# Kernel optimization log

Measured on AMD Instinct MI355X. Metric: run time of the kernel, lower is better.

## Reference

```python
import jax, jax.numpy as jnp
import numpy as np

B, L, D, S = 4, 4096, 1024, 16
EPS = 1e-5  # nn.LayerNorm default


def setup_inputs() -> dict:
    key = jax.random.key(0)
    ks = jax.random.split(key, 8)
    s = 0.02
    return {
        "x_seq": jax.random.normal(ks[0], (B, L, D), jnp.float32),
        "h_prev": jnp.zeros((B, S), jnp.float32),
        "gamma": jnp.ones((D,), jnp.float32),
        "beta": jnp.zeros((D,), jnp.float32),
        "W_in": jax.random.normal(ks[1], (D, D), jnp.float32) * s,
        "b_in": jnp.zeros((D,), jnp.float32),
        "W_A": jax.random.normal(ks[2], (D, S), jnp.float32) * s,
        "b_A": jnp.zeros((S,), jnp.float32),
        "W_B": jax.random.normal(ks[3], (D, S), jnp.float32) * s,
        "b_B": jnp.zeros((S,), jnp.float32),
        "W_C": jax.random.normal(ks[4], (D, S), jnp.float32) * s,
        "b_C": jnp.zeros((S,), jnp.float32),
        "W_dt": jax.random.normal(ks[5], (D, 1), jnp.float32) * s,
        "b_dt": jnp.zeros((1,), jnp.float32),
        "W_out": jax.random.normal(ks[6], (D, D), jnp.float32) * s,
        "b_out": jnp.zeros((D,), jnp.float32),
    }


def _layernorm(x, gamma, beta):
    mu = jnp.mean(x, axis=-1, keepdims=True)
    var = jnp.mean(jnp.square(x - mu), axis=-1, keepdims=True)
    return (x - mu) * jax.lax.rsqrt(var + EPS) * gamma + beta


def reference(x_seq, h_prev, gamma, beta, W_in, b_in, W_A, b_A, W_B, b_B,
              W_C, b_C, W_dt, b_dt, W_out, b_out):
    # pre-scan projections (all batched over (B, L))
    x = _layernorm(x_seq, gamma, beta)
    x = jax.nn.silu(x @ W_in + b_in)                    # (B, L, D)
    log_A = -jax.nn.softplus(x @ W_A + b_A)             # (B, L, S)
    B_t = x @ W_B + b_B                                 # (B, L, S)
    C_t = x @ W_C + b_C                                 # (B, L, S)
    dt = jax.nn.softplus(x @ W_dt + b_dt)               # (B, L, 1)
    A_disc = jnp.exp(log_A * dt)                        # (B, L, S)
    u = jnp.mean(x, axis=-1, keepdims=True)             # (B, L, 1)
    Bu = (B_t * dt) * u                                 # (B, L, S)

    # selective scan: h_t = A_t * h_{t-1} + Bu_t  over time axis
    def step(h, inp):
        a_t, bu_t = inp
        h = a_t * h + bu_t
        return h, h

    h_final, hs = jax.lax.scan(
        step, h_prev,
        (jnp.swapaxes(A_disc, 0, 1), jnp.swapaxes(Bu, 0, 1)))
    hs = jnp.swapaxes(hs, 0, 1)                         # (B, L, S)

    y = jnp.sum(C_t * hs, axis=-1, keepdims=True)       # (B, L, 1)
    y_seq = (x * y) @ W_out + b_out + x_seq             # (B, L, D)
    return y_seq, h_final
```

## Files before the change

kernel.cpp:

```cpp
#include <hip/hip_runtime.h>

typedef unsigned short u16;
typedef unsigned int u32;
typedef __attribute__((ext_vector_type(8))) short short8;
typedef __attribute__((ext_vector_type(4))) float f32x4;

#define B_ 4
#define L_ 4096
#define D_ 1024
#define S_ 16
#define M_ (B_ * L_)

__device__ __forceinline__ float b2f(u16 h) {
    unsigned u = ((unsigned)h) << 16;
    return __builtin_bit_cast(float, u);
}
__device__ __forceinline__ u16 f2b(float f) {
    unsigned u = __builtin_bit_cast(unsigned, f);
    u += 0x7fffu + ((u >> 16) & 1u);
    return (u16)(u >> 16);
}
__device__ __forceinline__ float softplus_f(float z) {
    return z > 20.f ? z : log1pf(__expf(z));
}
__device__ __forceinline__ void gload16(const u16* g, const u16* l) {
    __builtin_amdgcn_global_load_lds(
        (const __attribute__((address_space(1))) u32*)g,
        (__attribute__((address_space(3))) u32*)l, 16, 0, 0);
}

__global__ __launch_bounds__(256) void transpose_to_bf16(
    const float* __restrict__ W0, u16* __restrict__ Wt0,
    const float* __restrict__ W1, u16* __restrict__ Wt1) {
    const float* W = blockIdx.z ? W1 : W0;
    u16* Wt = blockIdx.z ? Wt1 : Wt0;
    __shared__ float t[32][33];
    int bx = blockIdx.x, by = blockIdx.y;
    int x = threadIdx.x;
    for (int j = threadIdx.y; j < 32; j += 8)
        t[j][x] = W[(size_t)(by * 32 + j) * D_ + bx * 32 + x];
    __syncthreads();
    for (int j = threadIdx.y; j < 32; j += 8)
        Wt[(size_t)(bx * 32 + j) * D_ + by * 32 + x] = f2b(t[x][j]);
}

__global__ __launch_bounds__(256) void pack_wp(
    const float* __restrict__ WA, const float* __restrict__ WB,
    const float* __restrict__ WC, const float* __restrict__ Wdt,
    u16* __restrict__ Wp) {
    int idx = blockIdx.x * 256 + threadIdx.x;
    int s = idx >> 10, k = idx & 1023;
    float v;
    if (s < 16)       v = WA[k * 16 + s];
    else if (s < 32)  v = WB[k * 16 + (s - 16)];
    else if (s < 48)  v = WC[k * 16 + (s - 32)];
    else if (s == 48) v = Wdt[k];
    else if (s == 49) v = 1.0f / 1024.0f;
    else              v = 0.f;
    Wp[idx] = f2b(v);
}

__global__ __launch_bounds__(256) void ln_kernel(
    const float* __restrict__ x, const float* __restrict__ gamma,
    const float* __restrict__ beta, u16* __restrict__ out) {
    int row = blockIdx.x, tid = threadIdx.x;
    const float4 v = *(const float4*)&x[(size_t)row * D_ + tid * 4];
    float s = v.x + v.y + v.z + v.w;
    float q = v.x * v.x + v.y * v.y + v.z * v.z + v.w * v.w;
    for (int o = 32; o > 0; o >>= 1) { s += __shfl_down(s, o); q += __shfl_down(q, o); }
    __shared__ float ss[4], qq[4];
    int w = tid >> 6, lane = tid & 63;
    if (lane == 0) { ss[w] = s; qq[w] = q; }
    __syncthreads();
    if (tid == 0) {
        float S = ss[0] + ss[1] + ss[2] + ss[3];
        float Q = qq[0] + qq[1] + qq[2] + qq[3];
        float mu = S * (1.f / D_);
        float var = Q * (1.f / D_) - mu * mu;
        ss[0] = mu; qq[0] = rsqrtf(var + 1e-5f);
    }
    __syncthreads();
    float mu = ss[0], rs = qq[0];
    const float4 gv = *(const float4*)&gamma[tid * 4];
    const float4 bv = *(const float4*)&beta[tid * 4];
    ushort4 o4;
    o4.x = f2b((v.x - mu) * rs * gv.x + bv.x);
    o4.y = f2b((v.y - mu) * rs * gv.y + bv.y);
    o4.z = f2b((v.z - mu) * rs * gv.z + bv.z);
    o4.w = f2b((v.w - mu) * rs * gv.w + bv.w);
    *(ushort4*)&out[(size_t)row * D_ + tid * 4] = o4;
}

template <int EPI>
__global__ __launch_bounds__(512, 1) void gemm256(
    const u16* __restrict__ A, const u16* __restrict__ Bt,
    const float* __restrict__ bias, const float* __restrict__ resid,
    const float* __restrict__ yrow,
    u16* __restrict__ outB, float* __restrict__ outF,
    int M, int N, int K, int nTileN) {
    __shared__ u16 sm[65536];
    const int TILES = K >> 6;

    int nwg = gridDim.x;
    int bid = blockIdx.x;
    int swz = (bid & 7) * (nwg >> 3) + (bid >> 3);
    int bx = swz % nTileN, by = swz / nTileN;
    int rowBase = by * 256, colBase = bx * 256;

    int tid = threadIdx.x;
    int lane = tid & 63, w = tid >> 6;
    int wr = w >> 2, wc = w & 3;
    int lr = lane & 15, lg = lane >> 4;
    const unsigned woff = (unsigned)((lr * 32 + lg * 8) ^ ((lr & 8) ? 16 : 0));

    int sub = w;
    int pos = sub >> 1;
    int kblk = sub & 1;
    int r = lane >> 2;
    int chunk = (lane & 3) ^ ((r & 8) ? 2 : 0);
    int rowoff = (pos & 1) * 16 + (pos >> 1) * 128;
    const u16* gAs = A  + (size_t)(rowBase + rowoff + r) * K + kblk * 32 + chunk * 8;
    const u16* gBs = Bt + (size_t)(colBase + rowoff + r) * K + kblk * 32 + chunk * 8;
    const unsigned ldst = (unsigned)(pos * 4096 + (sub & 1) * 512 + (lane & 63) * 0);
    const unsigned subb = (unsigned)sub * 512u;

#define STAGEPAIR(tau, p)                                                        \
    do {                                                                         \
        unsigned _bb = (unsigned)((tau) & 1) * 32768u;                           \
        size_t _go = (size_t)(p) * 32 * K + (size_t)(tau) * 64;                  \
        gload16(gBs + _go, &sm[_bb + 16384u + (unsigned)(p) * 4096u + subb]);    \
        gload16(gAs + _go, &sm[_bb + (unsigned)(p) * 4096u + subb]);             \
    } while (0)

    f32x4 acc[8][4] = {};

    STAGEPAIR(0, 0); STAGEPAIR(0, 1); STAGEPAIR(0, 2); STAGEPAIR(0, 3);
    if (TILES > 1) { STAGEPAIR(1, 0); STAGEPAIR(1, 1); STAGEPAIR(1, 2); }
    asm volatile("s_waitcnt vmcnt(6)" ::: "memory");
    __builtin_amdgcn_s_barrier();

    for (int t = 0; t < TILES; ++t) {
        const unsigned bb = (unsigned)(t & 1) * 32768u;
        short8 bfr[4][2], afr[2][2];
#pragma unroll
        for (int n = 0; n < 4; n++) {
            int rb = wc * 4 + n;
            unsigned bo = bb + 16384u + (unsigned)(((rb & 7) >> 1)) * 4096u
                        + (unsigned)(((rb & 1) + ((rb >> 3) << 1)) << 1) * 512u + woff;
            bfr[n][0] = *(const short8*)&sm[bo];
            bfr[n][1] = *(const short8*)&sm[bo + 512u];
        }
#pragma unroll
        for (int dm = 0; dm < 2; dm++) {
            unsigned ao = bb + (unsigned)((dm + (wr << 1)) << 1) * 512u + woff;
            afr[dm][0] = *(const short8*)&sm[ao];
            afr[dm][1] = *(const short8*)&sm[ao + 512u];
        }
        if (t + 1 < TILES) STAGEPAIR(t + 1, 3);
        __builtin_amdgcn_s_barrier();
        __builtin_amdgcn_s_setprio(1);
#pragma unroll
        for (int dm = 0; dm < 2; dm++)
#pragma unroll
            for (int n = 0; n < 4; n++)
#pragma unroll
                for (int ks = 0; ks < 2; ks++)
                    acc[dm][n] = __builtin_amdgcn_mfma_f32_16x16x32_bf16(
                        afr[dm][ks], bfr[n][ks], acc[dm][n], 0, 0, 0);
        __builtin_amdgcn_s_setprio(0);
        __builtin_amdgcn_s_barrier();
#pragma unroll
        for (int q = 1; q < 4; q++) {
#pragma unroll
            for (int dm = 0; dm < 2; dm++) {
                int m = q * 2 + dm;
                unsigned ao = bb + (unsigned)q * 4096u
                            + (unsigned)(((m & 1) + (wr << 1)) << 1) * 512u + woff;
                afr[dm][0] = *(const short8*)&sm[ao];
                afr[dm][1] = *(const short8*)&sm[ao + 512u];
            }
            if (t + 2 < TILES) STAGEPAIR(t + 2, q - 1);
            __builtin_amdgcn_s_barrier();
            __builtin_amdgcn_s_setprio(1);
#pragma unroll
            for (int dm = 0; dm < 2; dm++)
#pragma unroll
                for (int n = 0; n < 4; n++)
#pragma unroll
                    for (int ks = 0; ks < 2; ks++)
                        acc[q * 2 + dm][n] = __builtin_amdgcn_mfma_f32_16x16x32_bf16(
                            afr[dm][ks], bfr[n][ks], acc[q * 2 + dm][n], 0, 0, 0);
            __builtin_amdgcn_s_setprio(0);
            if (q == 3) {
                if (t + 2 < TILES)      asm volatile("s_waitcnt vmcnt(6)" ::: "memory");
                else if (t + 1 < TILES) asm volatile("s_waitcnt vmcnt(0)" ::: "memory");
            }
            __builtin_amdgcn_s_barrier();
        }
    }
#undef STAGEPAIR

#pragma unroll
    for (int m = 0; m < 8; m++) {
        float yr[4];
        if (EPI == 2) {
#pragma unroll
            for (int j = 0; j < 4; j++)
                yr[j] = yrow[rowBase + wr * 128 + m * 16 + lg * 4 + j];
        }
#pragma unroll
        for (int n = 0; n < 4; n++)
#pragma unroll
            for (int j = 0; j < 4; j++) {
                int row = rowBase + wr * 128 + m * 16 + lg * 4 + j;
                int col = colBase + wc * 64 + n * 16 + lr;
                size_t o = (size_t)row * N + col;
                if (EPI == 1) {
                    float v = acc[m][n][j] + bias[col];
                    v = v / (1.f + __expf(-v));
                    outB[o] = f2b(v);
                } else {
                    outF[o] = acc[m][n][j] * yr[j] + bias[col] + resid[o];
                }
            }
    }
}

__global__ __launch_bounds__(256) void proj_kernel(
    const u16* __restrict__ X, const u16* __restrict__ Wp,
    const float* __restrict__ bA, const float* __restrict__ bB,
    const float* __restrict__ bC, const float* __restrict__ bdt,
    float* __restrict__ Ad, float* __restrict__ Bu, float* __restrict__ Ct) {
    __shared__ u16 Xs[64][32];
    __shared__ u16 Ws[64][32];
    int rowBase = blockIdx.x * 64;
    int tid = threadIdx.x, lane = tid & 63, w = tid >> 6;
    int lr = lane & 15, lg = lane >> 4;
    f32x4 acc[4] = {};
    int r0 = tid >> 2, c0 = (tid & 3) * 8;
    for (int k0 = 0; k0 < 1024; k0 += 32) {
        *(uint4*)&Xs[r0][c0] = *(const uint4*)&X[(size_t)(rowBase + r0) * 1024 + k0 + c0];
        *(uint4*)&Ws[r0][c0] = *(const uint4*)&Wp[(size_t)r0 * 1024 + k0 + c0];
        __syncthreads();
        short8 a = *(const short8*)&Xs[w * 16 + lr][lg * 8];
#pragma unroll
        for (int n = 0; n < 4; n++) {
            short8 b = *(const short8*)&Ws[n * 16 + lr][lg * 8];
            acc[n] = __builtin_amdgcn_mfma_f32_16x16x32_bf16(a, b, acc[n], 0, 0, 0);
        }
        __syncthreads();
    }
    float bdt0 = bdt[0];
#pragma unroll
    for (int j = 0; j < 4; j++) {
        int row = rowBase + w * 16 + lg * 4 + j;
        float dtr = __shfl(acc[3][j], lg * 16 + 0, 64);
        float uv  = __shfl(acc[3][j], lg * 16 + 1, 64);
        float dt = softplus_f(dtr + bdt0);
        float zA = acc[0][j] + bA[lr];
        float zB = acc[1][j] + bB[lr];
        float zC = acc[2][j] + bC[lr];
        size_t o = (size_t)row * 16 + lr;
        Ad[o] = __expf(-dt * softplus_f(zA));
        Bu[o] = zB * dt * uv;
        Ct[o] = zC;
    }
}

__global__ __launch_bounds__(1024) void scan_kernel(
    const float* __restrict__ Ad, const float* __restrict__ Bu,
    const float* __restrict__ Ct, const float* __restrict__ hprev,
    float* __restrict__ y, float* __restrict__ hfinal) {
    int b = blockIdx.x;
    int tid = threadIdx.x;
    int s = tid & 15, c = tid >> 4;
    const size_t base = (size_t)b * L_ * S_;
    float P = 1.f, Q = 0.f;
    for (int i = 0; i < 64; i++) {
        size_t idx = base + (size_t)(c * 64 + i) * S_ + s;
        float a = Ad[idx], bu = Bu[idx];
        P = a * P;
        Q = a * Q + bu;
    }
    __shared__ float Ps[16][64], Qs[16][64], Hin[16][65];
    Ps[s][c] = P; Qs[s][c] = Q;
    __syncthreads();
    if (tid < 16) {
        float h = hprev[b * S_ + tid];
        for (int cc = 0; cc < 64; cc++) {
            Hin[tid][cc] = h;
            h = Ps[tid][cc] * h + Qs[tid][cc];
        }
        hfinal[b * S_ + tid] = h;
    }
    __syncthreads();
    float h = Hin[s][c];
    for (int i = 0; i < 64; i++) {
        size_t idx = base + (size_t)(c * 64 + i) * S_ + s;
        h = Ad[idx] * h + Bu[idx];
        float p = Ct[idx] * h;
        p += __shfl_xor(p, 1);
        p += __shfl_xor(p, 2);
        p += __shfl_xor(p, 4);
        p += __shfl_xor(p, 8);
        if (s == 0) y[(size_t)b * L_ + c * 64 + i] = p;
    }
}

extern "C" void kernel_launch(void* const* d_in, const int* in_sizes, int n_in,
                              void* d_out, int out_size, void* d_ws, size_t ws_size,
                              hipStream_t stream) {
    const float* x_seq  = (const float*)d_in[0];
    const float* h_prev = (const float*)d_in[1];
    const float* gamma  = (const float*)d_in[2];
    const float* beta   = (const float*)d_in[3];
    const float* W_in   = (const float*)d_in[4];
    const float* b_in   = (const float*)d_in[5];
    const float* W_A    = (const float*)d_in[6];
    const float* b_A    = (const float*)d_in[7];
    const float* W_B    = (const float*)d_in[8];
    const float* b_B    = (const float*)d_in[9];
    const float* W_C    = (const float*)d_in[10];
    const float* b_C    = (const float*)d_in[11];
    const float* W_dt   = (const float*)d_in[12];
    const float* b_dt   = (const float*)d_in[13];
    const float* W_out  = (const float*)d_in[14];
    const float* b_out  = (const float*)d_in[15];

    char* ws = (char*)d_ws;
    u16*   x_ln   = (u16*)(ws + 0);
    u16*   x      = (u16*)(ws + 33554432);
    u16*   Wt_in  = (u16*)(ws + 67108864);
    u16*   Wt_out = (u16*)(ws + 69206016);
    u16*   Wp     = (u16*)(ws + 71303168);
    float* Ad     = (float*)(ws + 71434240);
    float* Bu     = (float*)(ws + 72482816);
    float* Ct     = (float*)(ws + 73531392);
    float* yv     = (float*)(ws + 74579968);
    float* out    = (float*)d_out;

    transpose_to_bf16<<<dim3(32, 32, 2), dim3(32, 8), 0, stream>>>(W_in, Wt_in, W_out, Wt_out);
    pack_wp<<<256, 256, 0, stream>>>(W_A, W_B, W_C, W_dt, Wp);
    ln_kernel<<<M_, 256, 0, stream>>>(x_seq, gamma, beta, x_ln);
    gemm256<1><<<(M_ / 256) * (D_ / 256), 512, 0, stream>>>(
        x_ln, Wt_in, b_in, nullptr, nullptr, x, nullptr, M_, D_, D_, D_ / 256);
    proj_kernel<<<M_ / 64, 256, 0, stream>>>(x, Wp, b_A, b_B, b_C, b_dt, Ad, Bu, Ct);
    scan_kernel<<<B_, 1024, 0, stream>>>(Ad, Bu, Ct, h_prev, yv, out + (size_t)M_ * D_);
    gemm256<2><<<(M_ / 256) * (D_ / 256), 512, 0, stream>>>(
        x, Wt_out, b_out, x_seq, yv, nullptr, out, M_, D_, D_, D_ / 256);
}
```

Before: 177.8 us.

## Parallelize scan across chunks, stage GEMM epilogue via LDS, pipeline proj loads

Replaces the 4-block scan with a three-kernel chunked scan over 256 blocks, so the sequential recurrence no longer runs on only four workgroups. The GEMM1 epilogue now writes bf16 results through swizzled LDS for coalesced 16-byte stores, and bias loads are hoisted. The projection kernel double-buffers its tiles with direct global-to-LDS loads, the GEMM issues its prefetch before the LDS fragment reads, and the two weight-prep kernels are merged into one launch. The extra scan kernels add launch overhead and a serial single-block middle pass.

```diff
diff --git a/kernel.cpp b/kernel.cpp
--- a/kernel.cpp
+++ b/kernel.cpp
@@ -10,6 +10,8 @@
 #define D_ 1024
 #define S_ 16
 #define M_ (B_ * L_)
+#define NBG 64
+#define LC 64
 
 __device__ __forceinline__ float b2f(u16 h) {
     unsigned u = ((unsigned)h) << 16;
@@ -29,35 +31,36 @@
         (__attribute__((address_space(3))) u32*)l, 16, 0, 0);
 }
 
-__global__ __launch_bounds__(256) void transpose_to_bf16(
+__global__ __launch_bounds__(256) void prep_kernel(
     const float* __restrict__ W0, u16* __restrict__ Wt0,
-    const float* __restrict__ W1, u16* __restrict__ Wt1) {
-    const float* W = blockIdx.z ? W1 : W0;
-    u16* Wt = blockIdx.z ? Wt1 : Wt0;
-    __shared__ float t[32][33];
-    int bx = blockIdx.x, by = blockIdx.y;
-    int x = threadIdx.x;
-    for (int j = threadIdx.y; j < 32; j += 8)
-        t[j][x] = W[(size_t)(by * 32 + j) * D_ + bx * 32 + x];
-    __syncthreads();
-    for (int j = threadIdx.y; j < 32; j += 8)
-        Wt[(size_t)(bx * 32 + j) * D_ + by * 32 + x] = f2b(t[x][j]);
-}
-
-__global__ __launch_bounds__(256) void pack_wp(
+    const float* __restrict__ W1, u16* __restrict__ Wt1,
     const float* __restrict__ WA, const float* __restrict__ WB,
     const float* __restrict__ WC, const float* __restrict__ Wdt,
     u16* __restrict__ Wp) {
-    int idx = blockIdx.x * 256 + threadIdx.x;
-    int s = idx >> 10, k = idx & 1023;
-    float v;
-    if (s < 16)       v = WA[k * 16 + s];
-    else if (s < 32)  v = WB[k * 16 + (s - 16)];
-    else if (s < 48)  v = WC[k * 16 + (s - 32)];
-    else if (s == 48) v = Wdt[k];
-    else if (s == 49) v = 1.0f / 1024.0f;
-    else              v = 0.f;
-    Wp[idx] = f2b(v);
+    int b = blockIdx.x, tid = threadIdx.x;
+    if (b < 2048) {
+        const float* W = (b >> 10) ? W1 : W0;
+        u16* Wt = (b >> 10) ? Wt1 : Wt0;
+        int by = (b >> 5) & 31, bx = b & 31;
+        int x = tid & 31, ty = tid >> 5;
+        __shared__ float t[32][33];
+        for (int j = ty; j < 32; j += 8)
+            t[j][x] = W[(size_t)(by * 32 + j) * D_ + bx * 32 + x];
+        __syncthreads();
+        for (int j = ty; j < 32; j += 8)
+            Wt[(size_t)(bx * 32 + j) * D_ + by * 32 + x] = f2b(t[x][j]);
+    } else {
+        int idx = (b - 2048) * 256 + tid;
+        int s = idx >> 10, k = idx & 1023;
+        float v;
+        if (s < 16)       v = WA[k * 16 + s];
+        else if (s < 32)  v = WB[k * 16 + (s - 16)];
+        else if (s < 48)  v = WC[k * 16 + (s - 32)];
+        else if (s == 48) v = Wdt[k];
+        else if (s == 49) v = 1.0f / 1024.0f;
+        else              v = 0.f;
+        Wp[idx] = f2b(v);
+    }
 }
 
 __global__ __launch_bounds__(256) void ln_kernel(
@@ -121,7 +124,6 @@
     int rowoff = (pos & 1) * 16 + (pos >> 1) * 128;
     const u16* gAs = A  + (size_t)(rowBase + rowoff + r) * K + kblk * 32 + chunk * 8;
     const u16* gBs = Bt + (size_t)(colBase + rowoff + r) * K + kblk * 32 + chunk * 8;
-    const unsigned ldst = (unsigned)(pos * 4096 + (sub & 1) * 512 + (lane & 63) * 0);
     const unsigned subb = (unsigned)sub * 512u;
 
 #define STAGEPAIR(tau, p)                                                        \
@@ -142,6 +144,7 @@
     for (int t = 0; t < TILES; ++t) {
         const unsigned bb = (unsigned)(t & 1) * 32768u;
         short8 bfr[4][2], afr[2][2];
+        if (t + 1 < TILES) STAGEPAIR(t + 1, 3);
 #pragma unroll
         for (int n = 0; n < 4; n++) {
             int rb = wc * 4 + n;
@@ -156,7 +159,6 @@
             afr[dm][0] = *(const short8*)&sm[ao];
             afr[dm][1] = *(const short8*)&sm[ao + 512u];
         }
-        if (t + 1 < TILES) STAGEPAIR(t + 1, 3);
         __builtin_amdgcn_s_barrier();
         __builtin_amdgcn_s_setprio(1);
 #pragma unroll
@@ -171,6 +173,7 @@
         __builtin_amdgcn_s_barrier();
 #pragma unroll
         for (int q = 1; q < 4; q++) {
+            if (t + 2 < TILES) STAGEPAIR(t + 2, q - 1);
 #pragma unroll
             for (int dm = 0; dm < 2; dm++) {
                 int m = q * 2 + dm;
@@ -179,7 +182,6 @@
                 afr[dm][0] = *(const short8*)&sm[ao];
                 afr[dm][1] = *(const short8*)&sm[ao + 512u];
             }
-            if (t + 2 < TILES) STAGEPAIR(t + 2, q - 1);
             __builtin_amdgcn_s_barrier();
             __builtin_amdgcn_s_setprio(1);
 #pragma unroll
@@ -200,29 +202,52 @@
     }
 #undef STAGEPAIR
 
-#pragma unroll
-    for (int m = 0; m < 8; m++) {
-        float yr[4];
-        if (EPI == 2) {
+    if (EPI == 1) {
+        float bcol[4];
+#pragma unroll
+        for (int n = 0; n < 4; n++) bcol[n] = bias[colBase + wc * 64 + n * 16 + lr];
+#pragma unroll
+        for (int m = 0; m < 8; m++)
+#pragma unroll
+            for (int n = 0; n < 4; n++)
+#pragma unroll
+                for (int j = 0; j < 4; j++) {
+                    int row = wr * 128 + m * 16 + lg * 4 + j;
+                    int col = wc * 64 + n * 16 + lr;
+                    float v = acc[m][n][j] + bcol[n];
+                    v = v / (1.f + __expf(-v));
+                    int cbs = (col >> 4) ^ lg;
+                    sm[row * 256 + cbs * 16 + (col & 15)] = f2b(v);
+                }
+        __syncthreads();
+        int rr = tid >> 1, half = tid & 1;
+        u16* gout = outB + (size_t)(rowBase + rr) * N + colBase;
+#pragma unroll
+        for (int q = 0; q < 8; q++) {
+            int cb = half * 8 + q;
+            int cbs = cb ^ ((rr >> 2) & 3);
+            *(uint4*)&gout[cb * 16] = *(const uint4*)&sm[rr * 256 + cbs * 16];
+        }
+    } else {
+        float bcol[4];
+#pragma unroll
+        for (int n = 0; n < 4; n++) bcol[n] = bias[colBase + wc * 64 + n * 16 + lr];
+#pragma unroll
+        for (int m = 0; m < 8; m++) {
+            float yr[4];
 #pragma unroll
             for (int j = 0; j < 4; j++)
                 yr[j] = yrow[rowBase + wr * 128 + m * 16 + lg * 4 + j];
-        }
-#pragma unroll
-        for (int n = 0; n < 4; n++)
-#pragma unroll
-            for (int j = 0; j < 4; j++) {
-                int row = rowBase + wr * 128 + m * 16 + lg * 4 + j;
-                int col = colBase + wc * 64 + n * 16 + lr;
-                size_t o = (size_t)row * N + col;
-                if (EPI == 1) {
-                    float v = acc[m][n][j] + bias[col];
-                    v = v / (1.f + __expf(-v));
-                    outB[o] = f2b(v);
-                } else {
-                    outF[o] = acc[m][n][j] * yr[j] + bias[col] + resid[o];
+#pragma unroll
+            for (int n = 0; n < 4; n++)
+#pragma unroll
+                for (int j = 0; j < 4; j++) {
+                    int row = rowBase + wr * 128 + m * 16 + lg * 4 + j;
+                    int col = colBase + wc * 64 + n * 16 + lr;
+                    size_t o = (size_t)row * N + col;
+                    outF[o] = acc[m][n][j] * yr[j] + bcol[n] + resid[o];
                 }
-            }
+        }
     }
 }
 
@@ -231,25 +256,37 @@
     const float* __restrict__ bA, const float* __restrict__ bB,
     const float* __restrict__ bC, const float* __restrict__ bdt,
     float* __restrict__ Ad, float* __restrict__ Bu, float* __restrict__ Ct) {
-    __shared__ u16 Xs[64][32];
-    __shared__ u16 Ws[64][32];
+    __shared__ u16 Xs[2][64][32];
+    __shared__ u16 Ws[2][64][32];
     int rowBase = blockIdx.x * 64;
     int tid = threadIdx.x, lane = tid & 63, w = tid >> 6;
     int lr = lane & 15, lg = lane >> 4;
     f32x4 acc[4] = {};
-    int r0 = tid >> 2, c0 = (tid & 3) * 8;
+    const int sr = lane >> 2, sc = (lane & 3) * 8;
+    const u16* gX = &X[(size_t)(rowBase + w * 16 + sr) * 1024 + sc];
+    const u16* gW = &Wp[(size_t)(w * 16 + sr) * 1024 + sc];
+
+#define PSTAGE(d, k0)                              \
+    do {                                           \
+        gload16(gX + (k0), &Xs[d][w * 16][0]);     \
+        gload16(gW + (k0), &Ws[d][w * 16][0]);     \
+    } while (0)
+
+    PSTAGE(0, 0);
+    __syncthreads();
+    int cur = 0;
     for (int k0 = 0; k0 < 1024; k0 += 32) {
-        *(uint4*)&Xs[r0][c0] = *(const uint4*)&X[(size_t)(rowBase + r0) * 1024 + k0 + c0];
-        *(uint4*)&Ws[r0][c0] = *(const uint4*)&Wp[(size_t)r0 * 1024 + k0 + c0];
+        if (k0 + 32 < 1024) PSTAGE(cur ^ 1, k0 + 32);
+        short8 a = *(const short8*)&Xs[cur][w * 16 + lr][lg * 8];
+#pragma unroll
+        for (int n = 0; n < 4; n++) {
+            short8 b = *(const short8*)&Ws[cur][n * 16 + lr][lg * 8];
+            acc[n] = __builtin_amdgcn_mfma_f32_16x16x32_bf16(a, b, acc[n], 0, 0, 0);
+        }
         __syncthreads();
-        short8 a = *(const short8*)&Xs[w * 16 + lr][lg * 8];
-#pragma unroll
-        for (int n = 0; n < 4; n++) {
-            short8 b = *(const short8*)&Ws[n * 16 + lr][lg * 8];
-            acc[n] = __builtin_amdgcn_mfma_f32_16x16x32_bf16(a, b, acc[n], 0, 0, 0);
-        }
-        __syncthreads();
-    }
+        cur ^= 1;
+    }
+#undef PSTAGE
     float bdt0 = bdt[0];
 #pragma unroll
     for (int j = 0; j < 4; j++) {
@@ -267,44 +304,71 @@
     }
 }
 
-__global__ __launch_bounds__(1024) void scan_kernel(
+__global__ __launch_bounds__(1024) void scan_part1(
     const float* __restrict__ Ad, const float* __restrict__ Bu,
-    const float* __restrict__ Ct, const float* __restrict__ hprev,
-    float* __restrict__ y, float* __restrict__ hfinal) {
-    int b = blockIdx.x;
+    float* __restrict__ Pb, float* __restrict__ Qb) {
+    int b = blockIdx.x >> 6, g = blockIdx.x & 63;
     int tid = threadIdx.x;
     int s = tid & 15, c = tid >> 4;
-    const size_t base = (size_t)b * L_ * S_;
-    float P = 1.f, Q = 0.f;
-    for (int i = 0; i < 64; i++) {
-        size_t idx = base + (size_t)(c * 64 + i) * S_ + s;
-        float a = Ad[idx], bu = Bu[idx];
-        P = a * P;
-        Q = a * Q + bu;
-    }
+    size_t idx = ((size_t)b * L_ + g * LC + c) * S_ + s;
+    float a = Ad[idx], bu = Bu[idx];
+    __shared__ float Ps[16][64], Qs[16][64];
+    Ps[s][c] = a; Qs[s][c] = bu;
+    __syncthreads();
+    if (tid < 16) {
+        float P = 1.f, Q = 0.f;
+        for (int cc = 0; cc < 64; cc++) {
+            float pa = Ps[tid][cc], qa = Qs[tid][cc];
+            P = pa * P;
+            Q = pa * Q + qa;
+        }
+        int o = (b * NBG + g) * S_ + tid;
+        Pb[o] = P; Qb[o] = Q;
+    }
+}
+
+__global__ __launch_bounds__(64) void scan_part2(
+    const float* __restrict__ Pb, const float* __restrict__ Qb,
+    const float* __restrict__ hprev, float* __restrict__ Hb,
+    float* __restrict__ hfinal) {
+    int t = threadIdx.x;
+    int b = t >> 4, s = t & 15;
+    float h = hprev[b * S_ + s];
+    for (int g = 0; g < NBG; g++) {
+        int o = (b * NBG + g) * S_ + s;
+        Hb[o] = h;
+        h = Pb[o] * h + Qb[o];
+    }
+    hfinal[b * S_ + s] = h;
+}
+
+__global__ __launch_bounds__(1024) void scan_part3(
+    const float* __restrict__ Ad, const float* __restrict__ Bu,
+    const float* __restrict__ Ct, const float* __restrict__ Hb,
+    float* __restrict__ y) {
+    int b = blockIdx.x >> 6, g = blockIdx.x & 63;
+    int tid = threadIdx.x;
+    int s = tid & 15, c = tid >> 4;
+    size_t idx = ((size_t)b * L_ + g * LC + c) * S_ + s;
+    float a = Ad[idx], bu = Bu[idx];
     __shared__ float Ps[16][64], Qs[16][64], Hin[16][65];
-    Ps[s][c] = P; Qs[s][c] = Q;
+    Ps[s][c] = a; Qs[s][c] = bu;
     __syncthreads();
     if (tid < 16) {
-        float h = hprev[b * S_ + tid];
+        float h = Hb[(b * NBG + g) * S_ + tid];
         for (int cc = 0; cc < 64; cc++) {
             Hin[tid][cc] = h;
             h = Ps[tid][cc] * h + Qs[tid][cc];
         }
-        hfinal[b * S_ + tid] = h;
-    }
-    __syncthreads();
-    float h = Hin[s][c];
-    for (int i = 0; i < 64; i++) {
-        size_t idx = base + (size_t)(c * 64 + i) * S_ + s;
-        h = Ad[idx] * h + Bu[idx];
-        float p = Ct[idx] * h;
-        p += __shfl_xor(p, 1);
-        p += __shfl_xor(p, 2);
-        p += __shfl_xor(p, 4);
-        p += __shfl_xor(p, 8);
-        if (s == 0) y[(size_t)b * L_ + c * 64 + i] = p;
-    }
+    }
+    __syncthreads();
+    float h = a * Hin[s][c] + bu;
+    float p = Ct[idx] * h;
+    p += __shfl_xor(p, 1);
+    p += __shfl_xor(p, 2);
+    p += __shfl_xor(p, 4);
+    p += __shfl_xor(p, 8);
+    if (s == 0) y[(size_t)b * L_ + g * LC + c] = p;
 }
 
 extern "C" void kernel_launch(void* const* d_in, const int* in_sizes, int n_in,
@@ -337,15 +401,20 @@
     float* Bu     = (float*)(ws + 72482816);
     float* Ct     = (float*)(ws + 73531392);
     float* yv     = (float*)(ws + 74579968);
+    float* Pb     = (float*)(ws + 74645504);
+    float* Qb     = (float*)(ws + 74661888);
+    float* Hb     = (float*)(ws + 74678272);
     float* out    = (float*)d_out;
 
-    transpose_to_bf16<<<dim3(32, 32, 2), dim3(32, 8), 0, stream>>>(W_in, Wt_in, W_out, Wt_out);
-    pack_wp<<<256, 256, 0, stream>>>(W_A, W_B, W_C, W_dt, Wp);
+    prep_kernel<<<2304, 256, 0, stream>>>(W_in, Wt_in, W_out, Wt_out,
+                                          W_A, W_B, W_C, W_dt, Wp);
     ln_kernel<<<M_, 256, 0, stream>>>(x_seq, gamma, beta, x_ln);
     gemm256<1><<<(M_ / 256) * (D_ / 256), 512, 0, stream>>>(
         x_ln, Wt_in, b_in, nullptr, nullptr, x, nullptr, M_, D_, D_, D_ / 256);
     proj_kernel<<<M_ / 64, 256, 0, stream>>>(x, Wp, b_A, b_B, b_C, b_dt, Ad, Bu, Ct);
-    scan_kernel<<<B_, 1024, 0, stream>>>(Ad, Bu, Ct, h_prev, yv, out + (size_t)M_ * D_);
+    scan_part1<<<B_ * NBG, 1024, 0, stream>>>(Ad, Bu, Pb, Qb);
+    scan_part2<<<1, 64, 0, stream>>>(Pb, Qb, h_prev, Hb, out + (size_t)M_ * D_);
+    scan_part3<<<B_ * NBG, 1024, 0, stream>>>(Ad, Bu, Ct, Hb, yv);
     gemm256<2><<<(M_ / 256) * (D_ / 256), 512, 0, stream>>>(
         x, Wt_out, b_out, x_seq, yv, nullptr, out, M_, D_, D_, D_ / 256);
 }
```

Measured after the change: 153.3 us. -13.8%, faster.
